# Optimization experiments

Measured on AMD Instinct MI355X. Metric: run time of the kernel, lower is better.

Reference implementation:

```python
import jax, jax.numpy as jnp
import numpy as np

N_NODES = 100000
N_EDGES = 1600000
N_GRAPHS = 64
D_IN = 128
D_HID = 128
D_OUT = 4
LEAKY_SLOPE = 0.01  # nn.LeakyReLU default


def setup_inputs() -> dict:
    key = jax.random.key(0)
    k1, k2, k3, k4, k5 = jax.random.split(key, 5)
    x = jax.random.normal(k1, (N_NODES, D_IN), dtype=jnp.float32)
    edge_index = jax.random.randint(k2, (2, N_EDGES), 0, N_NODES, dtype=jnp.int32)
    batch = jnp.sort(jax.random.randint(k3, (N_NODES,), 0, N_GRAPHS, dtype=jnp.int32))
    s1 = 1.0 / np.sqrt(D_IN)
    W1 = jax.random.uniform(k4, (D_IN, D_HID), jnp.float32, -s1, s1)
    b1 = jnp.zeros((D_HID,), jnp.float32)
    W2 = jax.random.uniform(k5, (D_HID, D_OUT), jnp.float32, -s1, s1)
    b2 = jnp.zeros((D_OUT,), jnp.float32)
    return {"x": x, "edge_index": edge_index, "batch": batch,
            "W1": W1, "b1": b1, "W2": W2, "b2": b2}


def _gcn_conv(x, src, dst, norm, W, b, n_nodes):
    # h = X W; messages = norm * h[src]; aggregate at dst; add bias
    h = x @ W
    msg = h[src] * norm[:, None]
    agg = jax.ops.segment_sum(msg, dst, num_segments=n_nodes)
    return agg + b


def reference(x, edge_index, batch, W1, b1, W2, b2):
    n = x.shape[0]
    # add self-loops (PyG GCNConv default)
    loops = jnp.arange(n, dtype=edge_index.dtype)
    src = jnp.concatenate([edge_index[0], loops])
    dst = jnp.concatenate([edge_index[1], loops])
    # symmetric normalization: deg over target index, weight 1
    deg = jax.ops.segment_sum(jnp.ones_like(src, dtype=x.dtype), dst, num_segments=n)
    deg_is = jnp.where(deg > 0, jax.lax.rsqrt(deg), 0.0)
    norm = deg_is[src] * deg_is[dst]

    h = _gcn_conv(x, src, dst, norm, W1, b1, n)
    h = jnp.where(h >= 0, h, LEAKY_SLOPE * h)  # LeakyReLU
    # dropout is identity at inference
    h = _gcn_conv(h, src, dst, norm, W2, b2, n)

    # global mean pool over graphs
    sums = jax.ops.segment_sum(h, batch, num_segments=N_GRAPHS)
    cnts = jax.ops.segment_sum(jnp.ones((n,), h.dtype), batch, num_segments=N_GRAPHS)
    pooled = sums / jnp.maximum(cnts, 1.0)[:, None]
    return jax.nn.softmax(pooled, axis=1)
```

## Files before the change

kernel.cpp:

```cpp
#include <hip/hip_runtime.h>

#define D 128
#define NG 64
#define NPB 128
#define MAXBK 1024
#define CAPB 4096
#define PCHUNK 2048
#define PLCAP 4608
#define LDA 136

typedef unsigned int uint;
typedef unsigned short ushort_t;
typedef unsigned char uchar_t;
typedef float v2f __attribute__((ext_vector_type(2)));
typedef short s8v __attribute__((ext_vector_type(8)));
typedef float f4v __attribute__((ext_vector_type(4)));

__device__ __forceinline__ uint bfr(float x) {
    uint u = __float_as_uint(x);
    return (u + 0x7FFFu + ((u >> 16) & 1u)) >> 16;
}

__global__ __launch_bounds__(256) void k_init(const float* __restrict__ W,
                                              short* __restrict__ W1T,
                                              int* __restrict__ gcur,
                                              float* __restrict__ psum,
                                              float* __restrict__ pcnt, int NBK) {
    int tid = threadIdx.x;
    int idx = blockIdx.x * 256 + tid;
    int nn = idx >> 7, kk = idx & 127;
    W1T[idx] = (short)bfr(W[kk * D + nn]);
    if (idx < NBK) gcur[idx] = idx * CAPB;
    if (blockIdx.x == 0) {
        psum[tid] = 0.f;
        if (tid < NG) pcnt[tid] = 0.f;
    }
}

__global__ __launch_bounds__(256) void k_part(const int* __restrict__ edge,
                                              int* __restrict__ gcur, int* __restrict__ p1,
                                              int E, int NBK) {
    __shared__ int hist[MAXBK], scn[MAXBK], curb[MAXBK], fixb[MAXBK];
    __shared__ int ps[256];
    __shared__ int sortb[PCHUNK];
    __shared__ ushort_t sbkt[PCHUNK];
    int tid = threadIdx.x;
    for (int i = tid; i < MAXBK; i += 256) { hist[i] = 0; curb[i] = 0; }
    __syncthreads();
    int lo = blockIdx.x * PCHUNK;
    int hi = min(lo + PCHUNK, E);
    int cnt = hi - lo;
    int4 dv[2], sv[2];
#pragma unroll
    for (int it = 0; it < 2; ++it) {
        int q = lo + tid * 4 + it * 1024;
        if (q + 4 <= hi) {
            dv[it] = *(const int4*)&edge[E + q];
            sv[it] = *(const int4*)&edge[q];
            atomicAdd(&hist[dv[it].x >> 7], 1);
            atomicAdd(&hist[dv[it].y >> 7], 1);
            atomicAdd(&hist[dv[it].z >> 7], 1);
            atomicAdd(&hist[dv[it].w >> 7], 1);
        } else {
            dv[it].x = (q + 0 < hi) ? edge[E + q + 0] : 0;
            dv[it].y = (q + 1 < hi) ? edge[E + q + 1] : 0;
            dv[it].z = (q + 2 < hi) ? edge[E + q + 2] : 0;
            dv[it].w = 0;
            sv[it].x = (q + 0 < hi) ? edge[q + 0] : 0;
            sv[it].y = (q + 1 < hi) ? edge[q + 1] : 0;
            sv[it].z = (q + 2 < hi) ? edge[q + 2] : 0;
            sv[it].w = 0;
            if (q + 0 < hi) atomicAdd(&hist[dv[it].x >> 7], 1);
            if (q + 1 < hi) atomicAdd(&hist[dv[it].y >> 7], 1);
            if (q + 2 < hi) atomicAdd(&hist[dv[it].z >> 7], 1);
        }
    }
    __syncthreads();
    int a = hist[4 * tid + 0], b = hist[4 * tid + 1];
    int c = hist[4 * tid + 2], d = hist[4 * tid + 3];
    int s4 = a + b + c + d;
    ps[tid] = s4;
    __syncthreads();
    for (int o = 1; o < 256; o <<= 1) {
        int x = (tid >= o) ? ps[tid - o] : 0;
        __syncthreads();
        ps[tid] += x;
        __syncthreads();
    }
    int pe = ps[tid] - s4;
    scn[4 * tid + 0] = pe;
    scn[4 * tid + 1] = pe + a;
    scn[4 * tid + 2] = pe + a + b;
    scn[4 * tid + 3] = pe + a + b + c;
    __syncthreads();
    for (int bk = tid; bk < NBK; bk += 256)
        if (hist[bk]) fixb[bk] = atomicAdd(&gcur[bk], hist[bk]) - scn[bk];
    __syncthreads();
#pragma unroll
    for (int it = 0; it < 2; ++it) {
        int q = lo + tid * 4 + it * 1024;
        {
            int d2 = dv[it].x, s = sv[it].x;
            if (q + 0 < hi) {
                int bk = d2 >> 7;
                int r = scn[bk] + atomicAdd(&curb[bk], 1);
                sortb[r] = ((d2 & 127) << 17) | s;
                sbkt[r] = (ushort_t)bk;
            }
        }
        {
            int d2 = dv[it].y, s = sv[it].y;
            if (q + 1 < hi) {
                int bk = d2 >> 7;
                int r = scn[bk] + atomicAdd(&curb[bk], 1);
                sortb[r] = ((d2 & 127) << 17) | s;
                sbkt[r] = (ushort_t)bk;
            }
        }
        {
            int d2 = dv[it].z, s = sv[it].z;
            if (q + 2 < hi) {
                int bk = d2 >> 7;
                int r = scn[bk] + atomicAdd(&curb[bk], 1);
                sortb[r] = ((d2 & 127) << 17) | s;
                sbkt[r] = (ushort_t)bk;
            }
        }
        {
            int d2 = dv[it].w, s = sv[it].w;
            if (q + 3 < hi) {
                int bk = d2 >> 7;
                int r = scn[bk] + atomicAdd(&curb[bk], 1);
                sortb[r] = ((d2 & 127) << 17) | s;
                sbkt[r] = (ushort_t)bk;
            }
        }
    }
    __syncthreads();
    for (int p = tid; p < cnt; p += 256) {
        int bk = sbkt[p];
        p1[fixb[bk] + p] = sortb[p];
    }
}

__global__ __launch_bounds__(256) void k_place(const int* __restrict__ p1,
                                               const int* __restrict__ gcur,
                                               int* __restrict__ ed, int2* __restrict__ offdeg,
                                               float* __restrict__ dinv, int n) {
    __shared__ int cnts[NPB], scn[NPB], cur[NPB];
    __shared__ int outb[PLCAP];
    __shared__ int tot;
    int tid = threadIdx.x;
    int b = blockIdx.x;
    int base = b * CAPB;
    int cnt = gcur[b] - base;
    int end = base + cnt;
    int node0 = b << 7;
    if (tid < NPB) { cnts[tid] = 0; cur[tid] = 0; }
    __syncthreads();
    int4 ev[4];
#pragma unroll
    for (int it = 0; it < 4; ++it) {
        int q = base + tid * 4 + it * 1024;
        ev[it] = *(const int4*)&p1[q];
        if (q + 4 <= end) {
            atomicAdd(&cnts[ev[it].x >> 17], 1);
            atomicAdd(&cnts[ev[it].y >> 17], 1);
            atomicAdd(&cnts[ev[it].z >> 17], 1);
            atomicAdd(&cnts[ev[it].w >> 17], 1);
        } else if (q < end) {
            atomicAdd(&cnts[ev[it].x >> 17], 1);
            if (q + 1 < end) atomicAdd(&cnts[ev[it].y >> 17], 1);
            if (q + 2 < end) atomicAdd(&cnts[ev[it].z >> 17], 1);
        }
    }
    __syncthreads();
    int v0 = 0, pc = 0;
    if (tid < NPB) {
        v0 = cnts[tid];
        pc = (v0 + 3) & ~3;
        scn[tid] = pc;
    }
    __syncthreads();
    for (int o = 1; o < NPB; o <<= 1) {
        int x = 0;
        if (tid < NPB && tid >= o) x = scn[tid - o];
        __syncthreads();
        if (tid < NPB) scn[tid] += x;
        __syncthreads();
    }
    if (tid == NPB - 1) tot = scn[NPB - 1];
    if (tid < NPB) {
        int excl = scn[tid] - pc;
        int node = node0 + tid;
        if (node < n) {
            offdeg[node] = make_int2(base + excl, v0);
            dinv[node] = rsqrtf((float)(v0 + 1));
        }
        scn[tid] = excl;
    }
    __syncthreads();
#pragma unroll
    for (int it = 0; it < 4; ++it) {
        int q = base + tid * 4 + it * 1024;
        {
            int v = ev[it].x;
            if (q + 0 < end) {
                int l = v >> 17;
                int r = scn[l] + atomicAdd(&cur[l], 1);
                if (r < PLCAP) outb[r] = v & 0x1FFFF;
            }
        }
        {
            int v = ev[it].y;
            if (q + 1 < end) {
                int l = v >> 17;
                int r = scn[l] + atomicAdd(&cur[l], 1);
                if (r < PLCAP) outb[r] = v & 0x1FFFF;
            }
        }
        {
            int v = ev[it].z;
            if (q + 2 < end) {
                int l = v >> 17;
                int r = scn[l] + atomicAdd(&cur[l], 1);
                if (r < PLCAP) outb[r] = v & 0x1FFFF;
            }
        }
        {
            int v = ev[it].w;
            if (q + 3 < end) {
                int l = v >> 17;
                int r = scn[l] + atomicAdd(&cur[l], 1);
                if (r < PLCAP) outb[r] = v & 0x1FFFF;
            }
        }
    }
    __syncthreads();
    int lim = (tot < PLCAP) ? tot : PLCAP;
    for (int p = tid; p < lim; p += 256) ed[base + p] = outb[p];
}

__global__ __launch_bounds__(256) void k_gemm_mfma(const float* __restrict__ X,
                                                   const short* __restrict__ W1T,
                                                   const float* __restrict__ dinv,
                                                   uchar_t* __restrict__ H8b, int M) {
    __shared__ short sA[128 * LDA];
    __shared__ short sB[128 * LDA];
    __shared__ float sDinv[128];
    const int tid = threadIdx.x;
    const int blockM = blockIdx.x * 128;

    if (tid < 128) {
        int gm = blockM + tid;
        sDinv[tid] = (gm < M) ? dinv[gm] : 0.f;
    }
    {
        int c = tid & 31, g = tid >> 5;
#pragma unroll
        for (int i = 0; i < 16; ++i) {
            int r = g + i * 8;
            int gm = blockM + r;
            float4 v = make_float4(0, 0, 0, 0);
            if (gm < M) v = *(const float4*)&X[(size_t)gm * D + c * 4];
            uint lo = bfr(v.x) | (bfr(v.y) << 16);
            uint hi = bfr(v.z) | (bfr(v.w) << 16);
            *(uint2*)&sA[r * LDA + c * 4] = make_uint2(lo, hi);
        }
    }
    {
        int nn = tid >> 1, seg = tid & 1;
        const short* src = W1T + nn * 128 + seg * 64;
        short* dst = &sB[nn * LDA + seg * 64];
#pragma unroll
        for (int i = 0; i < 8; ++i)
            *(int4*)&dst[i * 8] = *(const int4*)&src[i * 8];
    }
    __syncthreads();

    const int wv = tid >> 6;
    const int lane = tid & 63;
    const int m0w = (wv >> 1) * 64, n0w = (wv & 1) * 64;
    const int mrow = lane & 15;
    const int quad = lane >> 4;

    f4v acc[4][4];
#pragma unroll
    for (int mi = 0; mi < 4; ++mi)
#pragma unroll
        for (int ni = 0; ni < 4; ++ni) acc[mi][ni] = (f4v)(0.f);

#pragma unroll
    for (int ks = 0; ks < 4; ++ks) {
        s8v af[4], bf[4];
#pragma unroll
        for (int mi = 0; mi < 4; ++mi)
            af[mi] = *(const s8v*)&sA[(m0w + mi * 16 + mrow) * LDA + ks * 32 + quad * 8];
#pragma unroll
        for (int ni = 0; ni < 4; ++ni)
            bf[ni] = *(const s8v*)&sB[(n0w + ni * 16 + mrow) * LDA + ks * 32 + quad * 8];
#pragma unroll
        for (int mi = 0; mi < 4; ++mi)
#pragma unroll
            for (int ni = 0; ni < 4; ++ni)
                acc[mi][ni] = __builtin_amdgcn_mfma_f32_16x16x32_bf16(af[mi], bf[ni], acc[mi][ni], 0, 0, 0);
    }

#pragma unroll
    for (int mi = 0; mi < 4; ++mi) {
#pragma unroll
        for (int r = 0; r < 4; ++r) {
            int lrow = m0w + mi * 16 + quad * 4 + r;
            int gm = blockM + lrow;
            if (gm >= M) continue;
            float di = sDinv[lrow];
#pragma unroll
            for (int ni = 0; ni < 4; ++ni) {
                int col = n0w + ni * 16 + mrow;
                float v = acc[mi][ni][r] * di;
                uint p = __builtin_amdgcn_cvt_pk_fp8_f32(v, v, 0u, false);
                H8b[(size_t)gm * 128 + col] = (uchar_t)(p & 0xFF);
            }
        }
    }
}

__device__ __forceinline__ void acc4(float& c0, float& c1, float& c2, float& c3, uint r) {
    v2f lo = __builtin_amdgcn_cvt_pk_f32_fp8(r, false);
    v2f hi = __builtin_amdgcn_cvt_pk_f32_fp8(r, true);
    c0 += lo.x; c1 += lo.y; c2 += hi.x; c3 += hi.y;
}

__global__ __launch_bounds__(256, 8) void k_gather(const uint* __restrict__ T,
                                                   const int2* __restrict__ offdeg,
                                                   const int* __restrict__ ed,
                                                   const float* __restrict__ dinv,
                                                   const float* __restrict__ b1,
                                                   const float* __restrict__ W2,
                                                   float4* __restrict__ zs,
                                                   int n) {
    int tid = threadIdx.x;
    int node = blockIdx.x * 8 + (tid >> 5);
    if (node >= n) return;
    int lane = tid & 31;
    const uint* Tl = T + lane;
    float di = dinv[node];
    float c0, c1, c2, c3;
    {
        uint h = Tl[node << 5];
        v2f lo = __builtin_amdgcn_cvt_pk_f32_fp8(h, false);
        v2f hi = __builtin_amdgcn_cvt_pk_f32_fp8(h, true);
        c0 = lo.x; c1 = lo.y; c2 = hi.x; c3 = hi.y;
    }
    int2 od = offdeg[node];
    int j = od.x, j1 = od.x + od.y;
    for (; j + 16 <= j1; j += 16) {
        int4 e0 = *(const int4*)&ed[j];
        int4 e1 = *(const int4*)&ed[j + 4];
        int4 e2 = *(const int4*)&ed[j + 8];
        int4 e3 = *(const int4*)&ed[j + 12];
        uint r0 = Tl[e0.x << 5], r1 = Tl[e0.y << 5], r2 = Tl[e0.z << 5], r3 = Tl[e0.w << 5];
        uint r4 = Tl[e1.x << 5], r5 = Tl[e1.y << 5], r6 = Tl[e1.z << 5], r7 = Tl[e1.w << 5];
        uint r8 = Tl[e2.x << 5], r9 = Tl[e2.y << 5], r10 = Tl[e2.z << 5], r11 = Tl[e2.w << 5];
        uint r12 = Tl[e3.x << 5], r13 = Tl[e3.y << 5], r14 = Tl[e3.z << 5], r15 = Tl[e3.w << 5];
        acc4(c0, c1, c2, c3, r0);  acc4(c0, c1, c2, c3, r1);
        acc4(c0, c1, c2, c3, r2);  acc4(c0, c1, c2, c3, r3);
        acc4(c0, c1, c2, c3, r4);  acc4(c0, c1, c2, c3, r5);
        acc4(c0, c1, c2, c3, r6);  acc4(c0, c1, c2, c3, r7);
        acc4(c0, c1, c2, c3, r8);  acc4(c0, c1, c2, c3, r9);
        acc4(c0, c1, c2, c3, r10); acc4(c0, c1, c2, c3, r11);
        acc4(c0, c1, c2, c3, r12); acc4(c0, c1, c2, c3, r13);
        acc4(c0, c1, c2, c3, r14); acc4(c0, c1, c2, c3, r15);
    }
    if (j + 8 <= j1) {
        int4 e0 = *(const int4*)&ed[j];
        int4 e1 = *(const int4*)&ed[j + 4];
        uint r0 = Tl[e0.x << 5], r1 = Tl[e0.y << 5], r2 = Tl[e0.z << 5], r3 = Tl[e0.w << 5];
        uint r4 = Tl[e1.x << 5], r5 = Tl[e1.y << 5], r6 = Tl[e1.z << 5], r7 = Tl[e1.w << 5];
        acc4(c0, c1, c2, c3, r0); acc4(c0, c1, c2, c3, r1);
        acc4(c0, c1, c2, c3, r2); acc4(c0, c1, c2, c3, r3);
        acc4(c0, c1, c2, c3, r4); acc4(c0, c1, c2, c3, r5);
        acc4(c0, c1, c2, c3, r6); acc4(c0, c1, c2, c3, r7);
        j += 8;
    }
    if (j + 4 <= j1) {
        int4 e0 = *(const int4*)&ed[j];
        uint r0 = Tl[e0.x << 5], r1 = Tl[e0.y << 5], r2 = Tl[e0.z << 5], r3 = Tl[e0.w << 5];
        acc4(c0, c1, c2, c3, r0); acc4(c0, c1, c2, c3, r1);
        acc4(c0, c1, c2, c3, r2); acc4(c0, c1, c2, c3, r3);
        j += 4;
    }
    for (; j < j1; ++j) {
        uint r = Tl[ed[j] << 5];
        acc4(c0, c1, c2, c3, r);
    }
    int f = lane * 4;
    float v0 = di * c0 + b1[f + 0];
    float v1 = di * c1 + b1[f + 1];
    float v2 = di * c2 + b1[f + 2];
    float v3 = di * c3 + b1[f + 3];
    v0 = v0 >= 0.f ? v0 : 0.01f * v0;
    v1 = v1 >= 0.f ? v1 : 0.01f * v1;
    v2 = v2 >= 0.f ? v2 : 0.01f * v2;
    v3 = v3 >= 0.f ? v3 : 0.01f * v3;
    const float4* W2v = (const float4*)W2;
    float4 w0 = W2v[f + 0], w1 = W2v[f + 1], w2 = W2v[f + 2], w3 = W2v[f + 3];
    float a0 = v0 * w0.x + v1 * w1.x + v2 * w2.x + v3 * w3.x;
    float a1 = v0 * w0.y + v1 * w1.y + v2 * w2.y + v3 * w3.y;
    float a2 = v0 * w0.z + v1 * w1.z + v2 * w2.z + v3 * w3.z;
    float a3 = v0 * w0.w + v1 * w1.w + v2 * w2.w + v3 * w3.w;
#pragma unroll
    for (int o = 16; o >= 1; o >>= 1) {
        a0 += __shfl_xor(a0, o);
        a1 += __shfl_xor(a1, o);
        a2 += __shfl_xor(a2, o);
        a3 += __shfl_xor(a3, o);
    }
    if (lane == 0) zs[node] = make_float4(di * a0, di * a1, di * a2, di * a3);
}

__global__ __launch_bounds__(256) void k_pool2(const int2* __restrict__ offdeg,
                                               const int* __restrict__ ed,
                                               const float4* __restrict__ zs,
                                               const float* __restrict__ dinv,
                                               const int* __restrict__ batch,
                                               float* __restrict__ psum, float* __restrict__ pcnt,
                                               int n) {
    __shared__ float ls[NG * 4];
    __shared__ float lc[NG];
    int tid = threadIdx.x;
    ls[tid] = 0.f;
    if (tid < NG) lc[tid] = 0.f;
    __syncthreads();
    int idx = blockIdx.x * 256 + tid;
    int node = idx >> 1, h = idx & 1;
    if (node < n) {
        int2 od = offdeg[node];
        int d = od.y;
        int qend = od.x + (d & ~3);
        float a0 = 0.f, a1 = 0.f, a2 = 0.f, a3 = 0.f;
        if (h == 0) {
            float4 z = zs[node];
            a0 = z.x; a1 = z.y; a2 = z.z; a3 = z.w;
            for (int j = qend; j < od.x + d; ++j) {
                float4 z2 = zs[ed[j]];
                a0 += z2.x; a1 += z2.y; a2 += z2.z; a3 += z2.w;
            }
        }
        for (int j = od.x + h * 4; j + 4 <= qend; j += 8) {
            int4 e = *(const int4*)&ed[j];
            float4 z0 = zs[e.x], z1 = zs[e.y], z2 = zs[e.z], z3 = zs[e.w];
            a0 += z0.x + z1.x + z2.x + z3.x;
            a1 += z0.y + z1.y + z2.y + z3.y;
            a2 += z0.z + z1.z + z2.z + z3.z;
            a3 += z0.w + z1.w + z2.w + z3.w;
        }
        a0 += __shfl_xor(a0, 1);
        a1 += __shfl_xor(a1, 1);
        a2 += __shfl_xor(a2, 1);
        a3 += __shfl_xor(a3, 1);
        if (h == 0) {
            float di = dinv[node];
            int g = batch[node];
            atomicAdd(&ls[g * 4 + 0], di * a0);
            atomicAdd(&ls[g * 4 + 1], di * a1);
            atomicAdd(&ls[g * 4 + 2], di * a2);
            atomicAdd(&ls[g * 4 + 3], di * a3);
            atomicAdd(&lc[g], 1.f);
        }
    }
    __syncthreads();
    atomicAdd(&psum[tid], ls[tid]);
    if (tid < NG) atomicAdd(&pcnt[tid], lc[tid]);
}

__global__ void k_final(const float* __restrict__ psum, const float* __restrict__ pcnt,
                        const float* __restrict__ b2, float* __restrict__ out) {
    int g = threadIdx.x;
    float c = fmaxf(pcnt[g], 1.f);
    float inv = 1.f / c;
    float l0 = psum[g * 4 + 0] * inv + b2[0];
    float l1 = psum[g * 4 + 1] * inv + b2[1];
    float l2 = psum[g * 4 + 2] * inv + b2[2];
    float l3 = psum[g * 4 + 3] * inv + b2[3];
    float m = fmaxf(fmaxf(l0, l1), fmaxf(l2, l3));
    float e0 = expf(l0 - m), e1 = expf(l1 - m), e2 = expf(l2 - m), e3 = expf(l3 - m);
    float s = 1.f / (e0 + e1 + e2 + e3);
    *(float4*)&out[g * 4] = make_float4(e0 * s, e1 * s, e2 * s, e3 * s);
}

extern "C" void kernel_launch(void* const* d_in, const int* in_sizes, int n_in,
                              void* d_out, int out_size, void* d_ws, size_t ws_size,
                              hipStream_t stream) {
    const float* X = (const float*)d_in[0];
    const int* edge = (const int*)d_in[1];
    const int* batch = (const int*)d_in[2];
    const float* W1 = (const float*)d_in[3];
    const float* b1 = (const float*)d_in[4];
    const float* W2 = (const float*)d_in[5];
    const float* b2 = (const float*)d_in[6];
    float* out = (float*)d_out;
    const int n = in_sizes[2];
    const int E = in_sizes[1] / 2;
    const int NBK = (n + NPB - 1) / NPB;

    uint* Hs = (uint*)d_ws;
    int* p1 = (int*)(Hs + (size_t)n * 32);
    int* ed = p1 + (size_t)NBK * CAPB;
    float4* zs = (float4*)(ed + (size_t)NBK * CAPB);
    float* dinv = (float*)(zs + n);
    int2* offdeg = (int2*)(dinv + n);
    short* W1T = (short*)(offdeg + n);
    int* gcur = (int*)(W1T + 16384);
    float* psum = (float*)(gcur + MAXBK);
    float* pcnt = psum + NG * 4;

    const int NP = (E + PCHUNK - 1) / PCHUNK;
    const int NGB = (n + 7) / 8;
    const int NPOOL = (2 * n + 255) / 256;

    k_init<<<64, 256, 0, stream>>>(W1, W1T, gcur, psum, pcnt, NBK);
    k_part<<<NP, 256, 0, stream>>>(edge, gcur, p1, E, NBK);
    k_place<<<NBK, 256, 0, stream>>>(p1, gcur, ed, offdeg, dinv, n);

    k_gemm_mfma<<<(n + 127) / 128, 256, 0, stream>>>(X, W1T, dinv, (uchar_t*)Hs, n);

    k_gather<<<NGB, 256, 0, stream>>>(Hs, offdeg, ed, dinv, b1, W2, zs, n);

    k_pool2<<<NPOOL, 256, 0, stream>>>(offdeg, ed, zs, dinv, batch, psum, pcnt, n);
    k_final<<<1, 64, 0, stream>>>(psum, pcnt, b2, out);
}
```

Before: 233.9 us.

## Build CSR with global atomic degree count, scan, and scatter instead of bucketed partition

Replaces the two-pass bucketed shared-memory partition (k_part/k_place) with a direct CSR build: a global atomic degree histogram, a per-block scan with an atomic global base, and an atomic-decrement scatter of source indices. This removes the fixed-capacity bucket buffers and the extra intermediate pass, but it relies on many random global atomics and leaves CSR segments non-contiguous in node order with non-deterministic edge order. The pooling kernel also now uses 4 lanes per node instead of 2.

```diff
diff --git a/kernel.cpp b/kernel.cpp
--- a/kernel.cpp
+++ b/kernel.cpp
@@ -2,15 +2,9 @@
 
 #define D 128
 #define NG 64
-#define NPB 128
-#define MAXBK 1024
-#define CAPB 4096
-#define PCHUNK 2048
-#define PLCAP 4608
 #define LDA 136
 
 typedef unsigned int uint;
-typedef unsigned short ushort_t;
 typedef unsigned char uchar_t;
 typedef float v2f __attribute__((ext_vector_type(2)));
 typedef short s8v __attribute__((ext_vector_type(8)));
@@ -23,222 +17,83 @@
 
 __global__ __launch_bounds__(256) void k_init(const float* __restrict__ W,
                                               short* __restrict__ W1T,
-                                              int* __restrict__ gcur,
+                                              int* __restrict__ deg,
+                                              int* __restrict__ gtotal,
                                               float* __restrict__ psum,
-                                              float* __restrict__ pcnt, int NBK) {
+                                              float* __restrict__ pcnt, int n) {
     int tid = threadIdx.x;
     int idx = blockIdx.x * 256 + tid;
     int nn = idx >> 7, kk = idx & 127;
     W1T[idx] = (short)bfr(W[kk * D + nn]);
-    if (idx < NBK) gcur[idx] = idx * CAPB;
+    for (int i = idx; i < n; i += 16384) deg[i] = 0;
     if (blockIdx.x == 0) {
         psum[tid] = 0.f;
         if (tid < NG) pcnt[tid] = 0.f;
-    }
-}
-
-__global__ __launch_bounds__(256) void k_part(const int* __restrict__ edge,
-                                              int* __restrict__ gcur, int* __restrict__ p1,
-                                              int E, int NBK) {
-    __shared__ int hist[MAXBK], scn[MAXBK], curb[MAXBK], fixb[MAXBK];
-    __shared__ int ps[256];
-    __shared__ int sortb[PCHUNK];
-    __shared__ ushort_t sbkt[PCHUNK];
+        if (tid == 0) *gtotal = 0;
+    }
+}
+
+__global__ __launch_bounds__(256) void k_deg(const int* __restrict__ edge,
+                                             int* __restrict__ deg, int E) {
+    int idx4 = (blockIdx.x * 256 + threadIdx.x) * 4;
+    if ((E & 3) == 0 && idx4 + 4 <= E) {
+        int4 d = *(const int4*)&edge[E + idx4];
+        atomicAdd(&deg[d.x], 1);
+        atomicAdd(&deg[d.y], 1);
+        atomicAdd(&deg[d.z], 1);
+        atomicAdd(&deg[d.w], 1);
+    } else {
+        int lim = (idx4 + 4 < E) ? idx4 + 4 : E;
+        for (int i = idx4; i < lim; ++i) atomicAdd(&deg[edge[E + i]], 1);
+    }
+}
+
+__global__ __launch_bounds__(256) void k_scan(const int* __restrict__ deg,
+                                              int2* __restrict__ offdeg,
+                                              float* __restrict__ dinv,
+                                              int* __restrict__ cur,
+                                              int* __restrict__ gtotal, int n) {
+    __shared__ int s[256];
+    __shared__ int sbase;
     int tid = threadIdx.x;
-    for (int i = tid; i < MAXBK; i += 256) { hist[i] = 0; curb[i] = 0; }
-    __syncthreads();
-    int lo = blockIdx.x * PCHUNK;
-    int hi = min(lo + PCHUNK, E);
-    int cnt = hi - lo;
-    int4 dv[2], sv[2];
-#pragma unroll
-    for (int it = 0; it < 2; ++it) {
-        int q = lo + tid * 4 + it * 1024;
-        if (q + 4 <= hi) {
-            dv[it] = *(const int4*)&edge[E + q];
-            sv[it] = *(const int4*)&edge[q];
-            atomicAdd(&hist[dv[it].x >> 7], 1);
-            atomicAdd(&hist[dv[it].y >> 7], 1);
-            atomicAdd(&hist[dv[it].z >> 7], 1);
-            atomicAdd(&hist[dv[it].w >> 7], 1);
-        } else {
-            dv[it].x = (q + 0 < hi) ? edge[E + q + 0] : 0;
-            dv[it].y = (q + 1 < hi) ? edge[E + q + 1] : 0;
-            dv[it].z = (q + 2 < hi) ? edge[E + q + 2] : 0;
-            dv[it].w = 0;
-            sv[it].x = (q + 0 < hi) ? edge[q + 0] : 0;
-            sv[it].y = (q + 1 < hi) ? edge[q + 1] : 0;
-            sv[it].z = (q + 2 < hi) ? edge[q + 2] : 0;
-            sv[it].w = 0;
-            if (q + 0 < hi) atomicAdd(&hist[dv[it].x >> 7], 1);
-            if (q + 1 < hi) atomicAdd(&hist[dv[it].y >> 7], 1);
-            if (q + 2 < hi) atomicAdd(&hist[dv[it].z >> 7], 1);
-        }
-    }
-    __syncthreads();
-    int a = hist[4 * tid + 0], b = hist[4 * tid + 1];
-    int c = hist[4 * tid + 2], d = hist[4 * tid + 3];
-    int s4 = a + b + c + d;
-    ps[tid] = s4;
+    int node = blockIdx.x * 256 + tid;
+    int d = (node < n) ? deg[node] : 0;
+    int pc = (d + 3) & ~3;
+    s[tid] = pc;
     __syncthreads();
     for (int o = 1; o < 256; o <<= 1) {
-        int x = (tid >= o) ? ps[tid - o] : 0;
+        int x = (tid >= o) ? s[tid - o] : 0;
         __syncthreads();
-        ps[tid] += x;
+        s[tid] += x;
         __syncthreads();
     }
-    int pe = ps[tid] - s4;
-    scn[4 * tid + 0] = pe;
-    scn[4 * tid + 1] = pe + a;
-    scn[4 * tid + 2] = pe + a + b;
-    scn[4 * tid + 3] = pe + a + b + c;
-    __syncthreads();
-    for (int bk = tid; bk < NBK; bk += 256)
-        if (hist[bk]) fixb[bk] = atomicAdd(&gcur[bk], hist[bk]) - scn[bk];
-    __syncthreads();
-#pragma unroll
-    for (int it = 0; it < 2; ++it) {
-        int q = lo + tid * 4 + it * 1024;
-        {
-            int d2 = dv[it].x, s = sv[it].x;
-            if (q + 0 < hi) {
-                int bk = d2 >> 7;
-                int r = scn[bk] + atomicAdd(&curb[bk], 1);
-                sortb[r] = ((d2 & 127) << 17) | s;
-                sbkt[r] = (ushort_t)bk;
-            }
-        }
-        {
-            int d2 = dv[it].y, s = sv[it].y;
-            if (q + 1 < hi) {
-                int bk = d2 >> 7;
-                int r = scn[bk] + atomicAdd(&curb[bk], 1);
-                sortb[r] = ((d2 & 127) << 17) | s;
-                sbkt[r] = (ushort_t)bk;
-            }
-        }
-        {
-            int d2 = dv[it].z, s = sv[it].z;
-            if (q + 2 < hi) {
-                int bk = d2 >> 7;
-                int r = scn[bk] + atomicAdd(&curb[bk], 1);
-                sortb[r] = ((d2 & 127) << 17) | s;
-                sbkt[r] = (ushort_t)bk;
-            }
-        }
-        {
-            int d2 = dv[it].w, s = sv[it].w;
-            if (q + 3 < hi) {
-                int bk = d2 >> 7;
-                int r = scn[bk] + atomicAdd(&curb[bk], 1);
-                sortb[r] = ((d2 & 127) << 17) | s;
-                sbkt[r] = (ushort_t)bk;
-            }
-        }
-    }
-    __syncthreads();
-    for (int p = tid; p < cnt; p += 256) {
-        int bk = sbkt[p];
-        p1[fixb[bk] + p] = sortb[p];
-    }
-}
-
-__global__ __launch_bounds__(256) void k_place(const int* __restrict__ p1,
-                                               const int* __restrict__ gcur,
-                                               int* __restrict__ ed, int2* __restrict__ offdeg,
-                                               float* __restrict__ dinv, int n) {
-    __shared__ int cnts[NPB], scn[NPB], cur[NPB];
-    __shared__ int outb[PLCAP];
-    __shared__ int tot;
-    int tid = threadIdx.x;
-    int b = blockIdx.x;
-    int base = b * CAPB;
-    int cnt = gcur[b] - base;
-    int end = base + cnt;
-    int node0 = b << 7;
-    if (tid < NPB) { cnts[tid] = 0; cur[tid] = 0; }
-    __syncthreads();
-    int4 ev[4];
-#pragma unroll
-    for (int it = 0; it < 4; ++it) {
-        int q = base + tid * 4 + it * 1024;
-        ev[it] = *(const int4*)&p1[q];
-        if (q + 4 <= end) {
-            atomicAdd(&cnts[ev[it].x >> 17], 1);
-            atomicAdd(&cnts[ev[it].y >> 17], 1);
-            atomicAdd(&cnts[ev[it].z >> 17], 1);
-            atomicAdd(&cnts[ev[it].w >> 17], 1);
-        } else if (q < end) {
-            atomicAdd(&cnts[ev[it].x >> 17], 1);
-            if (q + 1 < end) atomicAdd(&cnts[ev[it].y >> 17], 1);
-            if (q + 2 < end) atomicAdd(&cnts[ev[it].z >> 17], 1);
-        }
-    }
-    __syncthreads();
-    int v0 = 0, pc = 0;
-    if (tid < NPB) {
-        v0 = cnts[tid];
-        pc = (v0 + 3) & ~3;
-        scn[tid] = pc;
-    }
-    __syncthreads();
-    for (int o = 1; o < NPB; o <<= 1) {
-        int x = 0;
-        if (tid < NPB && tid >= o) x = scn[tid - o];
-        __syncthreads();
-        if (tid < NPB) scn[tid] += x;
-        __syncthreads();
-    }
-    if (tid == NPB - 1) tot = scn[NPB - 1];
-    if (tid < NPB) {
-        int excl = scn[tid] - pc;
-        int node = node0 + tid;
-        if (node < n) {
-            offdeg[node] = make_int2(base + excl, v0);
-            dinv[node] = rsqrtf((float)(v0 + 1));
-        }
-        scn[tid] = excl;
-    }
-    __syncthreads();
-#pragma unroll
-    for (int it = 0; it < 4; ++it) {
-        int q = base + tid * 4 + it * 1024;
-        {
-            int v = ev[it].x;
-            if (q + 0 < end) {
-                int l = v >> 17;
-                int r = scn[l] + atomicAdd(&cur[l], 1);
-                if (r < PLCAP) outb[r] = v & 0x1FFFF;
-            }
-        }
-        {
-            int v = ev[it].y;
-            if (q + 1 < end) {
-                int l = v >> 17;
-                int r = scn[l] + atomicAdd(&cur[l], 1);
-                if (r < PLCAP) outb[r] = v & 0x1FFFF;
-            }
-        }
-        {
-            int v = ev[it].z;
-            if (q + 2 < end) {
-                int l = v >> 17;
-                int r = scn[l] + atomicAdd(&cur[l], 1);
-                if (r < PLCAP) outb[r] = v & 0x1FFFF;
-            }
-        }
-        {
-            int v = ev[it].w;
-            if (q + 3 < end) {
-                int l = v >> 17;
-                int r = scn[l] + atomicAdd(&cur[l], 1);
-                if (r < PLCAP) outb[r] = v & 0x1FFFF;
-            }
-        }
-    }
-    __syncthreads();
-    int lim = (tot < PLCAP) ? tot : PLCAP;
-    for (int p = tid; p < lim; p += 256) ed[base + p] = outb[p];
+    int excl = s[tid] - pc;
+    if (tid == 255) sbase = atomicAdd(gtotal, s[255]);
+    __syncthreads();
+    if (node < n) {
+        int st = sbase + excl;
+        offdeg[node] = make_int2(st, d);
+        dinv[node] = rsqrtf((float)(d + 1));
+        cur[node] = st + d;
+    }
+}
+
+__global__ __launch_bounds__(256) void k_scatter(const int* __restrict__ edge,
+                                                 int* __restrict__ cur,
+                                                 int* __restrict__ ed, int E) {
+    int idx4 = (blockIdx.x * 256 + threadIdx.x) * 4;
+    if ((E & 3) == 0 && idx4 + 4 <= E) {
+        int4 dv = *(const int4*)&edge[E + idx4];
+        int4 sv = *(const int4*)&edge[idx4];
+        ed[atomicSub(&cur[dv.x], 1) - 1] = sv.x;
+        ed[atomicSub(&cur[dv.y], 1) - 1] = sv.y;
+        ed[atomicSub(&cur[dv.z], 1) - 1] = sv.z;
+        ed[atomicSub(&cur[dv.w], 1) - 1] = sv.w;
+    } else {
+        int lim = (idx4 + 4 < E) ? idx4 + 4 : E;
+        for (int i = idx4; i < lim; ++i)
+            ed[atomicSub(&cur[edge[E + i]], 1) - 1] = edge[i];
+    }
 }
 
 __global__ __launch_bounds__(256) void k_gemm_mfma(const float* __restrict__ X,
@@ -432,41 +287,48 @@
     ls[tid] = 0.f;
     if (tid < NG) lc[tid] = 0.f;
     __syncthreads();
-    int idx = blockIdx.x * 256 + tid;
-    int node = idx >> 1, h = idx & 1;
-    if (node < n) {
-        int2 od = offdeg[node];
-        int d = od.y;
-        int qend = od.x + (d & ~3);
-        float a0 = 0.f, a1 = 0.f, a2 = 0.f, a3 = 0.f;
-        if (h == 0) {
-            float4 z = zs[node];
-            a0 = z.x; a1 = z.y; a2 = z.z; a3 = z.w;
-            for (int j = qend; j < od.x + d; ++j) {
-                float4 z2 = zs[ed[j]];
-                a0 += z2.x; a1 += z2.y; a2 += z2.z; a3 += z2.w;
-            }
-        }
-        for (int j = od.x + h * 4; j + 4 <= qend; j += 8) {
-            int4 e = *(const int4*)&ed[j];
-            float4 z0 = zs[e.x], z1 = zs[e.y], z2 = zs[e.z], z3 = zs[e.w];
-            a0 += z0.x + z1.x + z2.x + z3.x;
-            a1 += z0.y + z1.y + z2.y + z3.y;
-            a2 += z0.z + z1.z + z2.z + z3.z;
-            a3 += z0.w + z1.w + z2.w + z3.w;
-        }
-        a0 += __shfl_xor(a0, 1);
-        a1 += __shfl_xor(a1, 1);
-        a2 += __shfl_xor(a2, 1);
-        a3 += __shfl_xor(a3, 1);
-        if (h == 0) {
-            float di = dinv[node];
-            int g = batch[node];
-            atomicAdd(&ls[g * 4 + 0], di * a0);
-            atomicAdd(&ls[g * 4 + 1], di * a1);
-            atomicAdd(&ls[g * 4 + 2], di * a2);
-            atomicAdd(&ls[g * 4 + 3], di * a3);
-            atomicAdd(&lc[g], 1.f);
+    int lane = tid & 3;
+#pragma unroll
+    for (int pass = 0; pass < 2; ++pass) {
+        int node = blockIdx.x * 128 + pass * 64 + (tid >> 2);
+        if (node < n) {
+            int2 od = offdeg[node];
+            int base = od.x, d = od.y;
+            float a0, a1, a2, a3;
+            if (lane == 0) {
+                float4 z = zs[node];
+                a0 = z.x; a1 = z.y; a2 = z.z; a3 = z.w;
+            } else {
+                a0 = a1 = a2 = a3 = 0.f;
+            }
+            int nq = d >> 2;
+            for (int q = lane; q < nq; q += 4) {
+                int4 e = *(const int4*)&ed[base + q * 4];
+                float4 z0 = zs[e.x], z1 = zs[e.y], z2 = zs[e.z], z3 = zs[e.w];
+                a0 += z0.x + z1.x + z2.x + z3.x;
+                a1 += z0.y + z1.y + z2.y + z3.y;
+                a2 += z0.z + z1.z + z2.z + z3.z;
+                a3 += z0.w + z1.w + z2.w + z3.w;
+            }
+            if (lane == 0) {
+                for (int j = base + (nq << 2); j < base + d; ++j) {
+                    float4 z = zs[ed[j]];
+                    a0 += z.x; a1 += z.y; a2 += z.z; a3 += z.w;
+                }
+            }
+            a0 += __shfl_xor(a0, 1); a1 += __shfl_xor(a1, 1);
+            a2 += __shfl_xor(a2, 1); a3 += __shfl_xor(a3, 1);
+            a0 += __shfl_xor(a0, 2); a1 += __shfl_xor(a1, 2);
+            a2 += __shfl_xor(a2, 2); a3 += __shfl_xor(a3, 2);
+            if (lane == 0) {
+                float di = dinv[node];
+                int g = batch[node];
+                atomicAdd(&ls[g * 4 + 0], di * a0);
+                atomicAdd(&ls[g * 4 + 1], di * a1);
+                atomicAdd(&ls[g * 4 + 2], di * a2);
+                atomicAdd(&ls[g * 4 + 3], di * a3);
+                atomicAdd(&lc[g], 1.f);
+            }
         }
     }
     __syncthreads();
@@ -502,31 +364,33 @@
     float* out = (float*)d_out;
     const int n = in_sizes[2];
     const int E = in_sizes[1] / 2;
-    const int NBK = (n + NPB - 1) / NPB;
 
     uint* Hs = (uint*)d_ws;
-    int* p1 = (int*)(Hs + (size_t)n * 32);
-    int* ed = p1 + (size_t)NBK * CAPB;
-    float4* zs = (float4*)(ed + (size_t)NBK * CAPB);
+    int* ed = (int*)(Hs + (size_t)n * 32);
+    float4* zs = (float4*)(ed + (size_t)E + 4 * (size_t)n);
     float* dinv = (float*)(zs + n);
     int2* offdeg = (int2*)(dinv + n);
     short* W1T = (short*)(offdeg + n);
-    int* gcur = (int*)(W1T + 16384);
-    float* psum = (float*)(gcur + MAXBK);
+    int* deg = (int*)(W1T + 16384);
+    int* cur = deg + n;
+    int* gtotal = cur + n;
+    float* psum = (float*)(gtotal + 4);
     float* pcnt = psum + NG * 4;
 
-    const int NP = (E + PCHUNK - 1) / PCHUNK;
+    const int NE4 = (E + 1023) / 1024;
+    const int NSC = (n + 255) / 256;
     const int NGB = (n + 7) / 8;
-    const int NPOOL = (2 * n + 255) / 256;
-
-    k_init<<<64, 256, 0, stream>>>(W1, W1T, gcur, psum, pcnt, NBK);
-    k_part<<<NP, 256, 0, stream>>>(edge, gcur, p1, E, NBK);
-    k_place<<<NBK, 256, 0, stream>>>(p1, gcur, ed, offdeg, dinv, n);
+    const int NPL = (n + 127) / 128;
+
+    k_init<<<64, 256, 0, stream>>>(W1, W1T, deg, gtotal, psum, pcnt, n);
+    k_deg<<<NE4, 256, 0, stream>>>(edge, deg, E);
+    k_scan<<<NSC, 256, 0, stream>>>(deg, offdeg, dinv, cur, gtotal, n);
+    k_scatter<<<NE4, 256, 0, stream>>>(edge, cur, ed, E);
 
     k_gemm_mfma<<<(n + 127) / 128, 256, 0, stream>>>(X, W1T, dinv, (uchar_t*)Hs, n);
 
     k_gather<<<NGB, 256, 0, stream>>>(Hs, offdeg, ed, dinv, b1, W2, zs, n);
 
-    k_pool2<<<NPOOL, 256, 0, stream>>>(offdeg, ed, zs, dinv, batch, psum, pcnt, n);
+    k_pool2<<<NPL, 256, 0, stream>>>(offdeg, ed, zs, dinv, batch, psum, pcnt, n);
     k_final<<<1, 64, 0, stream>>>(psum, pcnt, b2, out);
 }
```

Result: slower. 392.3 us (+67.7%).
